# Kernel optimization log

Measured on AMD Instinct MI355X. Metric: run time of the kernel, lower is better.

Reference implementation:

```python
import jax, jax.numpy as jnp
import numpy as np

G = 32; N = G * G          # gridsize, num_nodes per graph
A = 16                      # n_agents
B = 32                      # batch_size
E = 4096                    # edges per graph (~4-neighbor grid)
F_IN = 16                   # input_dim
H = 64                      # hidden_dim
L = 3                       # n_graph_layers
MID = F_IN + L * H          # 208
CAT = 2 * MID + H           # 480
MIN_VAL = -1e8


def _layer_norm(x, g, b, eps=1e-5):
    m = x.mean(-1, keepdims=True)
    v = x.var(-1, keepdims=True)
    return (x - m) * jax.lax.rsqrt(v + eps) * g + b


def setup_inputs() -> dict:
    key = jax.random.key(0)
    ks = jax.random.split(key, 16)
    inp = {}
    inp["graph_nodes"] = jax.random.normal(ks[0], (B, N, F_IN), jnp.float32)
    inp["graph_edge_links"] = jax.random.randint(ks[1], (B, 2, E), 0, N)
    inp["agent_locations"] = jax.random.randint(ks[2], (B, A), 0, N)
    inp["mask"] = jax.random.bernoulli(ks[3], 0.5, (B, A * N))
    inp["dist_matrix"] = jax.random.uniform(ks[4], (N, N), jnp.float32)
    dims = [F_IN] + [H] * L
    k = 5
    for l in range(L):
        inp[f"conv{l}_W"] = jax.random.normal(ks[k], (dims[l], H), jnp.float32) * 0.05
        inp[f"conv{l}_b"] = jnp.zeros((H,), jnp.float32)
        inp[f"conv{l}_g"] = jnp.ones((H,), jnp.float32)
        inp[f"conv{l}_beta"] = jnp.zeros((H,), jnp.float32)
        k += 1
    inp["edges_W"] = jax.random.normal(ks[k], (1, H), jnp.float32) * 0.05
    inp["edges_b"] = jnp.zeros((H,), jnp.float32)
    inp["actor1_W"] = jax.random.normal(ks[k + 1], (CAT, MID), jnp.float32) * 0.05
    inp["actor1_b"] = jnp.zeros((MID,), jnp.float32)
    inp["bn_g"] = jnp.ones((MID,), jnp.float32)
    inp["bn_b"] = jnp.zeros((MID,), jnp.float32)
    inp["actor2_W"] = jax.random.normal(ks[k + 2], (MID, 1), jnp.float32) * 0.05
    inp["actor2_b"] = jnp.zeros((1,), jnp.float32)
    return inp


def reference(graph_nodes, graph_edge_links, agent_locations, mask, dist_matrix,
              conv0_W, conv0_b, conv0_g, conv0_beta,
              conv1_W, conv1_b, conv1_g, conv1_beta,
              conv2_W, conv2_b, conv2_g, conv2_beta,
              edges_W, edges_b, actor1_W, actor1_b, bn_g, bn_b,
              actor2_W, actor2_b):
    # --- batch graphs: offset node indices per graph (Batch.from_data_list) ---
    x = graph_nodes.reshape(B * N, F_IN)
    offs = (jnp.arange(B) * N)[:, None, None]
    ei = (graph_edge_links + offs).transpose(1, 0, 2).reshape(2, B * E)
    src, dst = ei[0], ei[1]

    conv_params = [(conv0_W, conv0_b, conv0_g, conv0_beta),
                   (conv1_W, conv1_b, conv1_g, conv1_beta),
                   (conv2_W, conv2_b, conv2_g, conv2_beta)]
    outs = [x]
    for W, bb, g, beta in conv_params:
        # GINConv with eps=-1: (1+eps)*x_i == 0, so out = mlp(sum_j x_j)
        agg = jax.ops.segment_sum(x[src], dst, num_segments=B * N)
        x = jax.nn.relu(_layer_norm(agg @ W + bb, g, beta))  # mlp relu; outer .relu() idempotent
        outs.append(x)
    xc = jnp.concatenate(outs, axis=1).reshape(B, N, MID)

    # --- all-pairs (agent, node) feature build ---
    a = jnp.take_along_axis(xc, agent_locations[:, :, None], axis=1)  # [B, A, MID]
    a = jnp.repeat(a, N, axis=1)                                      # [B, A*N, MID]
    bfeat = jnp.tile(xc, (1, A, 1))                                   # [B, A*N, MID]
    c = dist_matrix[agent_locations].reshape(B, A * N, 1)             # [B, A*N, 1]
    c = c @ edges_W + edges_b                                         # [B, A*N, H]
    h = jnp.concatenate([a, bfeat, c], axis=2).reshape(-1, CAT)

    h = h @ actor1_W + actor1_b
    mu = h.mean(0)
    var = h.var(0)
    h = (h - mu) * jax.lax.rsqrt(var + 1e-5) * bn_g + bn_b  # BatchNorm1d, training stats
    h = jax.nn.relu(h)
    logits = (h @ actor2_W + actor2_b).reshape(B, A * N)
    logits = jnp.where(mask, logits, MIN_VAL)
    return jax.nn.softmax(logits, axis=1)
```

## Files before the change

kernel.cpp:

```cpp
#include <hip/hip_runtime.h>
#include <cstddef>

#define B_    32
#define N_    1024
#define E_    4096
#define A_    16
#define FIN_  16
#define H_    64
#define MID_  208
#define NODES (B_ * N_)
#define NEDGE (B_ * E_)
#define ROWS  (B_ * A_ * N_)
#define AN_   (A_ * N_)

__device__ __forceinline__ float readlane_f(float v, int l) {
  return __uint_as_float(__builtin_amdgcn_readlane(__float_as_uint(v), l));
}

typedef __attribute__((ext_vector_type(8))) __bf16 bf16x8;
typedef __attribute__((ext_vector_type(4))) float f32x4;

__device__ __forceinline__ f32x4 mfma16(bf16x8 a, bf16x8 b, f32x4 c) {
  return __builtin_amdgcn_mfma_f32_16x16x32_bf16(a, b, c, 0, 0, 0);
}

__device__ __forceinline__ void cvt8(const float* __restrict__ p, bf16x8& hi, bf16x8& lo) {
  float4 v0 = *(const float4*)p;
  float4 v1 = *(const float4*)(p + 4);
  float vv[8] = {v0.x, v0.y, v0.z, v0.w, v1.x, v1.y, v1.z, v1.w};
#pragma unroll
  for (int i = 0; i < 8; i++) {
    __bf16 h = (__bf16)vv[i];
    hi[i] = h;
    lo[i] = (__bf16)(vv[i] - (float)h);
  }
}

__global__ __launch_bounds__(256) void k_front(const int* __restrict__ el,
                                               const float* __restrict__ dist,
                                               const int* __restrict__ loc,
                                               const float* __restrict__ W1,
                                               const float* __restrict__ eW,
                                               const float* __restrict__ eb,
                                               const float* __restrict__ b1,
                                               int* __restrict__ rowptr,
                                               int* __restrict__ counts,
                                               int* __restrict__ ssrc,
                                               float* __restrict__ d1row,
                                               float* __restrict__ c2row,
                                               float* __restrict__ e1,
                                               float* __restrict__ cu,
                                               float* __restrict__ base,
                                               __bf16* __restrict__ W1BTh,
                                               __bf16* __restrict__ W1BTl) {
  __shared__ int cnt[1024];
  __shared__ int cur[1024];
  __shared__ int part[256];
  __shared__ int ssrcS[4096];
  __shared__ int loc_s[16];
  int blk = blockIdx.x, t = threadIdx.x;
  if (blk < 32) {
    int b = blk;
    for (int i = t; i < 1024; i += 256) cnt[i] = 0;
    __syncthreads();
    const int* srcp = el + b * (2 * E_);
    const int* dstp = srcp + E_;
    for (int i = t; i < E_; i += 256) atomicAdd(&cnt[dstp[i]], 1);
    __syncthreads();
    int4 c4 = *(const int4*)&cnt[t * 4];
    int s = c4.x + c4.y + c4.z + c4.w;
    part[t] = s;
    __syncthreads();
    for (int off = 1; off < 256; off <<= 1) {
      int v = (t >= off) ? part[t - off] : 0;
      __syncthreads();
      part[t] += v;
      __syncthreads();
    }
    int prev = (t == 0) ? 0 : part[t - 1];
    int p0 = prev, p1 = p0 + c4.x, p2 = p1 + c4.y, p3 = p2 + c4.z;
    *(int4*)&rowptr[b * 1024 + t * 4] = make_int4(p0 + b * E_, p1 + b * E_, p2 + b * E_, p3 + b * E_);
    *(int4*)&counts[b * 1024 + t * 4] = c4;
    cur[t * 4 + 0] = p0;
    cur[t * 4 + 1] = p1;
    cur[t * 4 + 2] = p2;
    cur[t * 4 + 3] = p3;
    __syncthreads();
    for (int i = t; i < E_; i += 256) {
      int dl = dstp[i];
      int sl = srcp[i];
      int pos = atomicAdd(&cur[dl], 1);
      ssrcS[pos] = b * N_ + sl;
    }
    __syncthreads();
    for (int i = t; i < E_; i += 256) ssrc[b * E_ + i] = ssrcS[i];
  } else if (blk < 288) {
    int lane = t & 63, w = t >> 6;
    int r = (blk - 32) * 4 + w;
    const float* dr = dist + (size_t)r * N_;
    float s = 0.f, c2 = 0.f;
#pragma unroll
    for (int k = 0; k < 16; k++) {
      float v = dr[lane + 64 * k];
      s += v;
      c2 = fmaf(v, v, c2);
    }
#pragma unroll
    for (int o = 32; o > 0; o >>= 1) { s += __shfl_xor(s, o); c2 += __shfl_xor(c2, o); }
    if (lane == 0) { d1row[r] = s; c2row[r] = c2; }
  } else if (blk < 320) {
    int b = blk - 288;
    if (t < 16) loc_s[t] = loc[b * 16 + t];
    __syncthreads();
    float e4[4] = {0.f, 0.f, 0.f, 0.f};
    for (int a = 0; a < 16; a++) {
      const float* dr = dist + (size_t)loc_s[a] * N_;
#pragma unroll
      for (int k = 0; k < 4; k++) e4[k] += dr[t + 256 * k];
    }
#pragma unroll
    for (int k = 0; k < 4; k++) e1[b * N_ + t + 256 * k] = e4[k];
  } else if (blk == 320) {
    int j = t;
    if (j < MID_) {
      float c = 0.f, bs = 0.f;
      for (int k = 0; k < H_; k++) {
        float w = W1[(2 * MID_ + k) * MID_ + j];
        c = fmaf(eW[k], w, c);
        bs = fmaf(eb[k], w, bs);
      }
      cu[j] = c;
      base[j] = bs + b1[j];
    }
  } else {
    int jr = blk - 321;
    if (t < 224) {
      float v = (t < MID_) ? W1[(size_t)(MID_ + t) * MID_ + jr] : 0.f;
      __bf16 h = (__bf16)v;
      W1BTh[jr * 224 + t] = h;
      W1BTl[jr * 224 + t] = (__bf16)(v - (float)h);
    }
  }
}

template <int FINT, bool COPYIN>
__global__ __launch_bounds__(256) void k_layer(const float* __restrict__ xin, int xstride, int in_off,
                                               float* __restrict__ xc, int out_off,
                                               const int* __restrict__ rowptr,
                                               const int* __restrict__ counts,
                                               const int* __restrict__ ssrc,
                                               const float* __restrict__ W,
                                               const float* __restrict__ bias,
                                               const float* __restrict__ g,
                                               const float* __restrict__ beta) {
  int t = threadIdx.x, lane = t & 63, w = t >> 6;
  float Wcol[FINT];
#pragma unroll
  for (int f = 0; f < FINT; f++) Wcol[f] = W[f * 64 + lane];
  float bv = bias[lane], gv = g[lane], bev = beta[lane];
  constexpr int CH = 64 / FINT;
  int f = lane & (FINT - 1);
  int ch = (FINT == 64) ? 0 : (lane >> 4);
  int blk = blockIdx.x;
  int xcd = blk & 7, kk = blk >> 3;
  int graph = xcd * 4 + (kk >> 5);
  int nblk = kk & 31;
  int nbase = graph * N_ + nblk * 32 + w * 8;

  float agg[8];
#pragma unroll
  for (int nn = 0; nn < 8; nn++) {
    int node = nbase + nn;
    int r0 = rowptr[node];
    int deg = counts[node];
    float a0 = 0.f, a1 = 0.f, a2 = 0.f, a3 = 0.f;
    int e = ch;
    for (; e + 3 * CH < deg; e += 4 * CH) {
      int s0 = ssrc[r0 + e];
      int s1 = ssrc[r0 + e + CH];
      int s2 = ssrc[r0 + e + 2 * CH];
      int s3 = ssrc[r0 + e + 3 * CH];
      a0 += xin[(size_t)s0 * xstride + in_off + f];
      a1 += xin[(size_t)s1 * xstride + in_off + f];
      a2 += xin[(size_t)s2 * xstride + in_off + f];
      a3 += xin[(size_t)s3 * xstride + in_off + f];
    }
    for (; e < deg; e += CH) {
      int s = ssrc[r0 + e];
      a0 += xin[(size_t)s * xstride + in_off + f];
    }
    agg[nn] = (a0 + a1) + (a2 + a3);
  }

#pragma unroll
  for (int nn = 0; nn < 8; nn++) {
    int node = nbase + nn;
    float aggf = agg[nn];
    float y0 = bv, y1 = 0.f, y2 = 0.f, y3 = 0.f;
#pragma unroll
    for (int l = 0; l < 64; l += 4) {
      y0 = fmaf(readlane_f(aggf, l + 0), Wcol[(l + 0) & (FINT - 1)], y0);
      y1 = fmaf(readlane_f(aggf, l + 1), Wcol[(l + 1) & (FINT - 1)], y1);
      y2 = fmaf(readlane_f(aggf, l + 2), Wcol[(l + 2) & (FINT - 1)], y2);
      y3 = fmaf(readlane_f(aggf, l + 3), Wcol[(l + 3) & (FINT - 1)], y3);
    }
    float y = (y0 + y1) + (y2 + y3);
    float m = y;
#pragma unroll
    for (int o = 32; o > 0; o >>= 1) m += __shfl_xor(m, o);
    m *= (1.f / 64.f);
    float d = y - m;
    float vv = d * d;
#pragma unroll
    for (int o = 32; o > 0; o >>= 1) vv += __shfl_xor(vv, o);
    vv *= (1.f / 64.f);
    float outv = fmaxf(d * rsqrtf(vv + 1e-5f) * gv + bev, 0.f);
    xc[(size_t)node * MID_ + out_off + lane] = outv;
    if (COPYIN) {
      if (lane < FIN_) xc[(size_t)node * MID_ + lane] = xin[(size_t)node * FIN_ + lane];
    }
  }
}

__global__ __launch_bounds__(256) void k_p1(const float* __restrict__ xc,
                                            const float* __restrict__ W1,
                                            const __bf16* __restrict__ W1BTh,
                                            const __bf16* __restrict__ W1BTl,
                                            const float* __restrict__ e1,
                                            const int* __restrict__ loc,
                                            float* __restrict__ pBT,
                                            float* __restrict__ pA,
                                            float* __restrict__ SB1,
                                            float* __restrict__ SB2,
                                            float* __restrict__ SB3) {
  __shared__ float xr[MID_];
  int t = threadIdx.x, lane = t & 63;
  int w = t >> 6;
  int blk = blockIdx.x;
  if (blk < 1024) {
    int nb = blk * 32;
    int q = lane >> 4, li = lane & 15;
    int jt0 = (w == 0) ? 0 : (w == 1) ? 4 : (w == 2) ? 7 : 10;
    int njt = (w == 0) ? 4 : 3;
    f32x4 zero4 = {0.f, 0.f, 0.f, 0.f};
    f32x4 acc0[4], acc1[4];
#pragma unroll
    for (int i = 0; i < 4; i++) { acc0[i] = zero4; acc1[i] = zero4; }
    const float* xr0 = xc + (size_t)(nb + li) * MID_;
    const float* xr1 = xc + (size_t)(nb + 16 + li) * MID_;
    for (int kc = 0; kc < 7; kc++) {
      int k0 = kc * 32 + q * 8;
      bf16x8 b0h, b0l, b1h, b1l;
      if (k0 < MID_) {
        cvt8(xr0 + k0, b0h, b0l);
        cvt8(xr1 + k0, b1h, b1l);
      } else {
#pragma unroll
        for (int i = 0; i < 8; i++) {
          b0h[i] = (__bf16)0.f; b0l[i] = (__bf16)0.f;
          b1h[i] = (__bf16)0.f; b1l[i] = (__bf16)0.f;
        }
      }
#pragma unroll
      for (int jj = 0; jj < 4; jj++) {
        if (jj < njt) {
          int jt = jt0 + jj;
          bf16x8 ah = *(const bf16x8*)(W1BTh + (size_t)(jt * 16 + li) * 224 + k0);
          bf16x8 al = *(const bf16x8*)(W1BTl + (size_t)(jt * 16 + li) * 224 + k0);
          acc0[jj] = mfma16(ah, b0h, acc0[jj]);
          acc0[jj] = mfma16(ah, b0l, acc0[jj]);
          acc0[jj] = mfma16(al, b0h, acc0[jj]);
          acc1[jj] = mfma16(ah, b1h, acc1[jj]);
          acc1[jj] = mfma16(ah, b1l, acc1[jj]);
          acc1[jj] = mfma16(al, b1h, acc1[jj]);
        }
      }
    }
    float ev0 = e1[nb + li];
    float ev1 = e1[nb + 16 + li];
#pragma unroll
    for (int jj = 0; jj < 4; jj++) {
      if (jj < njt) {
        int jt = jt0 + jj;
#pragma unroll
        for (int r = 0; r < 4; r++) {
          int j = jt * 16 + q * 4 + r;
          float* pb = pBT + (size_t)j * NODES + nb + li;
          pb[0] = acc0[jj][r];
          pb[16] = acc1[jj][r];
        }
        float s1v[4], s2v[4], s3v[4];
#pragma unroll
        for (int r = 0; r < 4; r++) {
          float a0 = acc0[jj][r], a1 = acc1[jj][r];
          s1v[r] = a0 + a1;
          s2v[r] = fmaf(a0, a0, a1 * a1);
          s3v[r] = fmaf(a0, ev0, a1 * ev1);
        }
#pragma unroll
        for (int o = 8; o > 0; o >>= 1) {
#pragma unroll
          for (int r = 0; r < 4; r++) {
            s1v[r] += __shfl_xor(s1v[r], o);
            s2v[r] += __shfl_xor(s2v[r], o);
            s3v[r] += __shfl_xor(s3v[r], o);
          }
        }
        if (li < 4) {
          float g1 = (li == 0) ? s1v[0] : (li == 1) ? s1v[1] : (li == 2) ? s1v[2] : s1v[3];
          float g2 = (li == 0) ? s2v[0] : (li == 1) ? s2v[1] : (li == 2) ? s2v[2] : s2v[3];
          float g3 = (li == 0) ? s3v[0] : (li == 1) ? s3v[1] : (li == 2) ? s3v[2] : s3v[3];
          int j = jt * 16 + q * 4 + li;
          SB1[(size_t)blk * MID_ + j] = g1;
          SB2[(size_t)blk * MID_ + j] = g2;
          SB3[(size_t)blk * MID_ + j] = g3;
        }
      }
    }
  } else {
    int ab = blk - 1024;
    int b = ab >> 4;
    int node = b * N_ + loc[ab];
    for (int i = t; i < MID_; i += 256) xr[i] = xc[(size_t)node * MID_ + i];
    __syncthreads();
    if (t < MID_) {
      float acc = 0.f;
      for (int i = 0; i < MID_; i++) acc = fmaf(xr[i], W1[i * MID_ + t], acc);
      pA[ab * MID_ + t] = acc;
    }
  }
}

__global__ __launch_bounds__(256) void k_fin(const float* __restrict__ SB1,
                                             const float* __restrict__ SB2,
                                             const float* __restrict__ SB3,
                                             const float* __restrict__ pA,
                                             const float* __restrict__ cu,
                                             const float* __restrict__ base,
                                             const float* __restrict__ d1row,
                                             const float* __restrict__ c2row,
                                             const int* __restrict__ loc,
                                             const float* __restrict__ bng,
                                             const float* __restrict__ bnb,
                                             const float* __restrict__ W2,
                                             float* __restrict__ vaT,
                                             float* __restrict__ wpack4) {
  __shared__ float utmp[1536 + 192];
  __shared__ float redm[4];
  __shared__ float reds[4];
  __shared__ float bcast[2];
  int t = threadIdx.x, lane = t & 63, w = t >> 6;
  int j = blockIdx.x;
  float cuj = cu[j], bj = base[j];
  float q1 = 0.f, q2 = 0.f, q3 = 0.f;
#pragma unroll
  for (int c = t * 4; c < t * 4 + 4; c++) {
    q1 += SB1[(size_t)c * MID_ + j];
    q2 += SB2[(size_t)c * MID_ + j];
    q3 += SB3[(size_t)c * MID_ + j];
  }
  float t1 = 0.f, t2 = 0.f, t3 = 0.f;
#pragma unroll
  for (int r = t * 2; r < t * 2 + 2; r++) {
    float pa = pA[r * MID_ + j] + bj;
    t1 += pa;
    t2 = fmaf(pa, pa, t2);
    t3 = fmaf(pa, d1row[loc[r]], t3);
  }
  utmp[0 * 256 + t] = q1;
  utmp[1 * 256 + t] = q2;
  utmp[2 * 256 + t] = q3;
  utmp[3 * 256 + t] = t1;
  utmp[4 * 256 + t] = t2;
  utmp[5 * 256 + t] = t3;
  float p1 = 0.f, p2 = 0.f;
#pragma unroll
  for (int r = t * 2; r < t * 2 + 2; r++) {
    int l = loc[r];
    p1 += d1row[l];
    p2 += c2row[l];
  }
#pragma unroll
  for (int o = 32; o > 0; o >>= 1) { p1 += __shfl_xor(p1, o); p2 += __shfl_xor(p2, o); }
  if (lane == 0) { redm[w] = p1; reds[w] = p2; }
  __syncthreads();
  if (t < 192) {
    int s = t >> 5, b32 = t & 31;
    float ssum = 0.f;
#pragma unroll
    for (int i = 0; i < 8; i++) ssum += utmp[s * 256 + b32 * 8 + i];
    utmp[1536 + s * 32 + b32] = ssum;
  }
  __syncthreads();
  if (t == 0) {
    float Sc1 = (redm[0] + redm[1]) + (redm[2] + redm[3]);
    float Sc2 = (reds[0] + reds[1]) + (reds[2] + reds[3]);
    double T1 = 0, T2 = 0, T3 = 0, cross = 0, sp1 = 0, sp2 = 0, spe = 0;
    for (int b = 0; b < 32; b++) {
      float sq1 = utmp[1536 + 0 * 32 + b];
      float sq2 = utmp[1536 + 1 * 32 + b];
      float sq3 = utmp[1536 + 2 * 32 + b];
      float pt1 = utmp[1536 + 3 * 32 + b];
      float pt2 = utmp[1536 + 4 * 32 + b];
      float pt3 = utmp[1536 + 5 * 32 + b];
      T1 += pt1; T2 += pt2; T3 += pt3;
      cross += (double)pt1 * sq1;
      sp1 += sq1; sp2 += sq2; spe += sq3;
    }
    double s1 = 1024.0 * T1 + 16.0 * sp1 + (double)cuj * Sc1;
    double s2 = 1024.0 * T2 + 16.0 * sp2 + (double)cuj * cuj * Sc2 +
                2.0 * (cross + (double)cuj * (T3 + spe));
    double mu = s1 * (1.0 / (double)ROWS);
    double var = s2 * (1.0 / (double)ROWS) - mu * mu;
    float sc = (float)(1.0 / sqrt(var + 1e-5)) * bng[j];
    float sh = bnb[j] - (float)mu * sc;
    bcast[0] = sc;
    bcast[1] = sh;
    wpack4[4 * j + 0] = sc;
    wpack4[4 * j + 1] = cuj * sc;
    wpack4[4 * j + 2] = W2[j];
    wpack4[4 * j + 3] = 0.f;
  }
  __syncthreads();
  float sc = bcast[0], sh = bcast[1];
#pragma unroll
  for (int r = t * 2; r < t * 2 + 2; r++) {
    int b = r >> 4, a = r & 15;
    float pa = pA[r * MID_ + j] + bj;
    vaT[((size_t)b * MID_ + j) * 16 + a] = pa * sc + sh;
  }
}

__global__ __launch_bounds__(512) void k_logits(const float* __restrict__ pBT,
                                                const float* __restrict__ vaT,
                                                const float* __restrict__ wpack4,
                                                const float* __restrict__ dist,
                                                const int* __restrict__ loc,
                                                const int* __restrict__ mask,
                                                const float* __restrict__ b2,
                                                float* __restrict__ lg,
                                                float2* __restrict__ Psm) {
  __shared__ float vaS[MID_ * 16];
  __shared__ float accL[8][8][64];
  __shared__ int loc_s[16];
  __shared__ float redm[8];
  __shared__ float reds[8];
  int t = threadIdx.x, lane = t & 63;
  int w = __builtin_amdgcn_readfirstlane(t >> 6);
  int b = blockIdx.y, nt = blockIdx.x;
  int n0 = nt * 64;
  if (t < 16) loc_s[t] = loc[b * 16 + t];
  for (int i = t; i < MID_ * 16; i += 512) vaS[i] = vaT[(size_t)b * MID_ * 16 + i];
  __syncthreads();
  float c[16];
#pragma unroll
  for (int a = 0; a < 16; a++) c[a] = dist[(size_t)loc_s[a] * N_ + n0 + lane];
  float acc16[16];
#pragma unroll
  for (int a = 0; a < 16; a++) acc16[a] = 0.f;
  const float4* wp = (const float4*)wpack4;
  int ng = b * N_ + n0 + lane;
  int jb = w * 26;
#pragma unroll 2
  for (int jj = 0; jj < 26; jj++) {
    int j = jb + jj;
    float pbv = pBT[(size_t)j * NODES + ng];
    float4 wv = wp[j];
    float pbs = pbv * wv.x;
    const float* va = &vaS[j * 16];
#pragma unroll
    for (int a = 0; a < 16; a++) {
      float h = fmaf(c[a], wv.y, va[a] + pbs);
      h = fmaxf(h, 0.f);
      acc16[a] = fmaf(h, wv.z, acc16[a]);
    }
  }

  float b2v = b2[0];
  float sv[2];
  int ois[2];
  unsigned mk = 0;
#pragma unroll
  for (int half = 0; half < 2; half++) {
#pragma unroll
    for (int a8 = 0; a8 < 8; a8++) accL[t >> 6][a8][lane] = acc16[half * 8 + a8];
    __syncthreads();
    {
      int a8 = t >> 6, nn = t & 63;
      float s = b2v;
#pragma unroll
      for (int ww = 0; ww < 8; ww++) s += accL[ww][a8][nn];
      int a = half * 8 + a8;
      int oi = b * AN_ + a * N_ + n0 + nn;
      bool m_ = mask[oi] != 0;
      sv[half] = m_ ? s : -1e8f;
      ois[half] = oi;
      mk |= (m_ ? 1u : 0u) << half;
    }
    __syncthreads();
  }

  float mx = fmaxf(sv[0], sv[1]);
#pragma unroll
  for (int o = 32; o > 0; o >>= 1) mx = fmaxf(mx, __shfl_xor(mx, o));
  if (lane == 0) redm[t >> 6] = mx;
  __syncthreads();
  mx = fmaxf(fmaxf(fmaxf(redm[0], redm[1]), fmaxf(redm[2], redm[3])),
             fmaxf(fmaxf(redm[4], redm[5]), fmaxf(redm[6], redm[7])));
  float ssum = 0.f;
#pragma unroll
  for (int iv = 0; iv < 2; iv++) {
    float pv = ((mk >> iv) & 1u) ? expf(sv[iv] - mx) : 0.f;
    lg[ois[iv]] = pv;
    ssum += pv;
  }
#pragma unroll
  for (int o = 32; o > 0; o >>= 1) ssum += __shfl_xor(ssum, o);
  if (lane == 0) reds[t >> 6] = ssum;
  __syncthreads();
  if (t == 0) {
    float S = ((reds[0] + reds[1]) + (reds[2] + reds[3])) +
              ((reds[4] + reds[5]) + (reds[6] + reds[7]));
    Psm[b * 16 + nt] = make_float2(mx, S);
  }
}

__global__ __launch_bounds__(256) void k_sm2(const float* __restrict__ lg,
                                             const float2* __restrict__ P,
                                             float* __restrict__ out) {
  __shared__ float scs[16];
  int b = blockIdx.y, x = blockIdx.x, t = threadIdx.x;
  float M = -3.0e38f;
  float2 pr[16];
#pragma unroll
  for (int k = 0; k < 16; k++) {
    pr[k] = P[b * 16 + k];
    M = fmaxf(M, pr[k].x);
  }
  float S = 0.f;
#pragma unroll
  for (int k = 0; k < 16; k++) S += pr[k].y * expf(pr[k].x - M);
  float inv = 1.0f / S;
  if (t < 16) scs[t] = expf(pr[t].x - M) * inv;
  __syncthreads();
  const float* lb = lg + b * AN_ + x * 2048;
  float* ob = out + b * AN_ + x * 2048;
#pragma unroll
  for (int k = 0; k < 8; k++) {
    int i = t + 256 * k;
    int n = (x * 2048 + i) & 1023;
    ob[i] = lb[i] * scs[n >> 6];
  }
}

extern "C" void kernel_launch(void* const* d_in, const int* in_sizes, int n_in,
                              void* d_out, int out_size, void* d_ws, size_t ws_size,
                              hipStream_t stream) {
  const float* gn = (const float*)d_in[0];
  const int* el = (const int*)d_in[1];
  const int* loc = (const int*)d_in[2];
  const int* mask = (const int*)d_in[3];
  const float* dist = (const float*)d_in[4];
  const float* c0W = (const float*)d_in[5];
  const float* c0b = (const float*)d_in[6];
  const float* c0g = (const float*)d_in[7];
  const float* c0be = (const float*)d_in[8];
  const float* c1W = (const float*)d_in[9];
  const float* c1b = (const float*)d_in[10];
  const float* c1g = (const float*)d_in[11];
  const float* c1be = (const float*)d_in[12];
  const float* c2W = (const float*)d_in[13];
  const float* c2b = (const float*)d_in[14];
  const float* c2g = (const float*)d_in[15];
  const float* c2be = (const float*)d_in[16];
  const float* eW = (const float*)d_in[17];
  const float* eb = (const float*)d_in[18];
  const float* W1 = (const float*)d_in[19];
  const float* b1 = (const float*)d_in[20];
  const float* bng = (const float*)d_in[21];
  const float* bnb = (const float*)d_in[22];
  const float* W2 = (const float*)d_in[23];
  const float* b2 = (const float*)d_in[24];
  float* out = (float*)d_out;

  char* p = (char*)d_ws;
  auto alloc = [&](size_t bytes) {
    char* r = p;
    p += (bytes + 255) & ~(size_t)255;
    return r;
  };
  int* counts = (int*)alloc((size_t)NODES * 4);
  int* rowptr = (int*)alloc((size_t)NODES * 4);
  int* ssrc = (int*)alloc((size_t)NEDGE * 4);
  float* xc = (float*)alloc((size_t)NODES * MID_ * 4);
  float* pBT = (float*)alloc((size_t)NODES * MID_ * 4);
  float* pA = (float*)alloc((size_t)512 * MID_ * 4);
  float* cu = (float*)alloc(256 * 4);
  float* base = (float*)alloc(256 * 4);
  float* d1row = (float*)alloc((size_t)N_ * 4);
  float* c2row = (float*)alloc((size_t)N_ * 4);
  float* e1 = (float*)alloc((size_t)B_ * N_ * 4);
  float* vaT = (float*)alloc((size_t)B_ * MID_ * 16 * 4);
  float* wpack4 = (float*)alloc((size_t)MID_ * 4 * 4);
  float* lg = (float*)alloc((size_t)ROWS * 4);
  float2* Psm = (float2*)alloc((size_t)B_ * 16 * 8);
  __bf16* W1BTh = (__bf16*)alloc((size_t)MID_ * 224 * 2);
  __bf16* W1BTl = (__bf16*)alloc((size_t)MID_ * 224 * 2);
  float* SB1 = (float*)alloc((size_t)1024 * MID_ * 4);
  float* SB2 = (float*)alloc((size_t)1024 * MID_ * 4);
  float* SB3 = (float*)alloc((size_t)1024 * MID_ * 4);

  k_front<<<529, 256, 0, stream>>>(el, dist, loc, W1, eW, eb, b1,
                                   rowptr, counts, ssrc, d1row, c2row, e1, cu, base,
                                   W1BTh, W1BTl);

  k_layer<16, true><<<1024, 256, 0, stream>>>(gn, FIN_, 0, xc, 16, rowptr, counts, ssrc, c0W, c0b, c0g, c0be);
  k_layer<64, false><<<1024, 256, 0, stream>>>(xc, MID_, 16, xc, 80, rowptr, counts, ssrc, c1W, c1b, c1g, c1be);
  k_layer<64, false><<<1024, 256, 0, stream>>>(xc, MID_, 80, xc, 144, rowptr, counts, ssrc, c2W, c2b, c2g, c2be);

  k_p1<<<1536, 256, 0, stream>>>(xc, W1, W1BTh, W1BTl, e1, loc, pBT, pA, SB1, SB2, SB3);
  k_fin<<<208, 256, 0, stream>>>(SB1, SB2, SB3, pA, cu, base, d1row, c2row, loc, bng, bnb, W2, vaT, wpack4);

  k_logits<<<dim3(16, 32), 512, 0, stream>>>(pBT, vaT, wpack4, dist, loc, mask, b2, lg, Psm);
  k_sm2<<<dim3(8, 32), 256, 0, stream>>>(lg, Psm, out);
}
```

Measured before the change: 246.1 us.

## Compute graph-layer dense transform with split-bf16 MFMA instead of readlane FMAs

The per-node 64x64 linear transform in the graph conv layers now runs as bf16 MFMA 16x16x32 with hi/lo splitting (three MFMAs per step) to keep near-fp32 accuracy. Before, each output used a chain of 64 readlane+FMA steps. Weights are transposed and split into bf16 hi/lo in extra k_front blocks. Aggregates are staged through shared memory, each wave now covers 16 nodes, and the grid is halved. LayerNorm and the output writes are vectorised. The cost is the shared staging, extra setup blocks and fewer blocks per layer, which may reduce latency hiding in the gather phase.

```diff
diff --git a/kernel.cpp b/kernel.cpp
--- a/kernel.cpp
+++ b/kernel.cpp
@@ -13,10 +13,6 @@
 #define ROWS  (B_ * A_ * N_)
 #define AN_   (A_ * N_)
 
-__device__ __forceinline__ float readlane_f(float v, int l) {
-  return __uint_as_float(__builtin_amdgcn_readlane(__float_as_uint(v), l));
-}
-
 typedef __attribute__((ext_vector_type(8))) __bf16 bf16x8;
 typedef __attribute__((ext_vector_type(4))) float f32x4;
 
@@ -43,6 +39,9 @@
                                                const float* __restrict__ eW,
                                                const float* __restrict__ eb,
                                                const float* __restrict__ b1,
+                                               const float* __restrict__ c0W,
+                                               const float* __restrict__ c1W,
+                                               const float* __restrict__ c2W,
                                                int* __restrict__ rowptr,
                                                int* __restrict__ counts,
                                                int* __restrict__ ssrc,
@@ -52,7 +51,9 @@
                                                float* __restrict__ cu,
                                                float* __restrict__ base,
                                                __bf16* __restrict__ W1BTh,
-                                               __bf16* __restrict__ W1BTl) {
+                                               __bf16* __restrict__ W1BTl,
+                                               __bf16* __restrict__ WTh,
+                                               __bf16* __restrict__ WTl) {
   __shared__ int cnt[1024];
   __shared__ int cur[1024];
   __shared__ int part[256];
@@ -132,7 +133,7 @@
       cu[j] = c;
       base[j] = bs + b1[j];
     }
-  } else {
+  } else if (blk < 529) {
     int jr = blk - 321;
     if (t < 224) {
       float v = (t < MID_) ? W1[(size_t)(MID_ + t) * MID_ + jr] : 0.f;
@@ -140,6 +141,17 @@
       W1BTh[jr * 224 + t] = h;
       W1BTl[jr * 224 + t] = (__bf16)(v - (float)h);
     }
+  } else {
+    int l = blk - 529;
+    const float* Wsrc = (l == 0) ? c0W : (l == 1) ? c1W : c2W;
+    int fmask = (l == 0) ? 15 : 63;
+    for (int i = t; i < 4096; i += 256) {
+      int j = i >> 6, k = i & 63;
+      float v = Wsrc[(k & fmask) * 64 + j];
+      __bf16 h = (__bf16)v;
+      WTh[l * 4096 + j * 64 + k] = h;
+      WTl[l * 4096 + j * 64 + k] = (__bf16)(v - (float)h);
+    }
   }
 }
 
@@ -149,28 +161,26 @@
                                                const int* __restrict__ rowptr,
                                                const int* __restrict__ counts,
                                                const int* __restrict__ ssrc,
-                                               const float* __restrict__ W,
+                                               const __bf16* __restrict__ WTh,
+                                               const __bf16* __restrict__ WTl,
                                                const float* __restrict__ bias,
                                                const float* __restrict__ g,
                                                const float* __restrict__ beta) {
+  __shared__ float aggS[4][16][68];
   int t = threadIdx.x, lane = t & 63, w = t >> 6;
-  float Wcol[FINT];
-#pragma unroll
-  for (int f = 0; f < FINT; f++) Wcol[f] = W[f * 64 + lane];
-  float bv = bias[lane], gv = g[lane], bev = beta[lane];
   constexpr int CH = 64 / FINT;
   int f = lane & (FINT - 1);
   int ch = (FINT == 64) ? 0 : (lane >> 4);
   int blk = blockIdx.x;
   int xcd = blk & 7, kk = blk >> 3;
-  int graph = xcd * 4 + (kk >> 5);
-  int nblk = kk & 31;
-  int nbase = graph * N_ + nblk * 32 + w * 8;
-
-  float agg[8];
-#pragma unroll
-  for (int nn = 0; nn < 8; nn++) {
-    int node = nbase + nn;
+  int graph = xcd * 4 + (kk >> 4);
+  int nblk = kk & 15;
+  int tilebase = graph * N_ + nblk * 64 + w * 16;
+
+  float aggv[16];
+#pragma unroll
+  for (int nn = 0; nn < 16; nn++) {
+    int node = tilebase + nn;
     int r0 = rowptr[node];
     int deg = counts[node];
     float a0 = 0.f, a1 = 0.f, a2 = 0.f, a3 = 0.f;
@@ -189,36 +199,72 @@
       int s = ssrc[r0 + e];
       a0 += xin[(size_t)s * xstride + in_off + f];
     }
-    agg[nn] = (a0 + a1) + (a2 + a3);
-  }
-
-#pragma unroll
-  for (int nn = 0; nn < 8; nn++) {
-    int node = nbase + nn;
-    float aggf = agg[nn];
-    float y0 = bv, y1 = 0.f, y2 = 0.f, y3 = 0.f;
-#pragma unroll
-    for (int l = 0; l < 64; l += 4) {
-      y0 = fmaf(readlane_f(aggf, l + 0), Wcol[(l + 0) & (FINT - 1)], y0);
-      y1 = fmaf(readlane_f(aggf, l + 1), Wcol[(l + 1) & (FINT - 1)], y1);
-      y2 = fmaf(readlane_f(aggf, l + 2), Wcol[(l + 2) & (FINT - 1)], y2);
-      y3 = fmaf(readlane_f(aggf, l + 3), Wcol[(l + 3) & (FINT - 1)], y3);
-    }
-    float y = (y0 + y1) + (y2 + y3);
-    float m = y;
-#pragma unroll
-    for (int o = 32; o > 0; o >>= 1) m += __shfl_xor(m, o);
-    m *= (1.f / 64.f);
-    float d = y - m;
-    float vv = d * d;
-#pragma unroll
-    for (int o = 32; o > 0; o >>= 1) vv += __shfl_xor(vv, o);
-    vv *= (1.f / 64.f);
-    float outv = fmaxf(d * rsqrtf(vv + 1e-5f) * gv + bev, 0.f);
-    xc[(size_t)node * MID_ + out_off + lane] = outv;
-    if (COPYIN) {
-      if (lane < FIN_) xc[(size_t)node * MID_ + lane] = xin[(size_t)node * FIN_ + lane];
-    }
+    aggv[nn] = (a0 + a1) + (a2 + a3);
+  }
+#pragma unroll
+  for (int nn = 0; nn < 16; nn++) aggS[w][nn][lane] = aggv[nn];
+
+  int q = lane >> 4, li = lane & 15;
+  bf16x8 bh[2], bl[2];
+#pragma unroll
+  for (int ks = 0; ks < 2; ks++) cvt8(&aggS[w][li][ks * 32 + q * 8], bh[ks], bl[ks]);
+
+  f32x4 zero4 = {0.f, 0.f, 0.f, 0.f};
+  f32x4 acc[4];
+#pragma unroll
+  for (int jt = 0; jt < 4; jt++) {
+    acc[jt] = zero4;
+#pragma unroll
+    for (int ks = 0; ks < 2; ks++) {
+      bf16x8 ah = *(const bf16x8*)(WTh + (size_t)(jt * 16 + li) * 64 + ks * 32 + q * 8);
+      bf16x8 al = *(const bf16x8*)(WTl + (size_t)(jt * 16 + li) * 64 + ks * 32 + q * 8);
+      acc[jt] = mfma16(ah, bh[ks], acc[jt]);
+      acc[jt] = mfma16(ah, bl[ks], acc[jt]);
+      acc[jt] = mfma16(al, bh[ks], acc[jt]);
+    }
+  }
+
+  float y[16];
+#pragma unroll
+  for (int jt = 0; jt < 4; jt++) {
+    float4 b4 = *(const float4*)(bias + jt * 16 + q * 4);
+    y[jt * 4 + 0] = acc[jt][0] + b4.x;
+    y[jt * 4 + 1] = acc[jt][1] + b4.y;
+    y[jt * 4 + 2] = acc[jt][2] + b4.z;
+    y[jt * 4 + 3] = acc[jt][3] + b4.w;
+  }
+  float s = 0.f;
+#pragma unroll
+  for (int i = 0; i < 16; i++) s += y[i];
+  s += __shfl_xor(s, 16);
+  s += __shfl_xor(s, 32);
+  float m = s * (1.f / 64.f);
+  float vv = 0.f;
+#pragma unroll
+  for (int i = 0; i < 16; i++) {
+    float d = y[i] - m;
+    vv = fmaf(d, d, vv);
+  }
+  vv += __shfl_xor(vv, 16);
+  vv += __shfl_xor(vv, 32);
+  float rs = rsqrtf(vv * (1.f / 64.f) + 1e-5f);
+
+  size_t node = tilebase + li;
+  float* xrow = xc + node * MID_ + out_off;
+#pragma unroll
+  for (int jt = 0; jt < 4; jt++) {
+    float4 g4 = *(const float4*)(g + jt * 16 + q * 4);
+    float4 be4 = *(const float4*)(beta + jt * 16 + q * 4);
+    float4 o;
+    o.x = fmaxf((y[jt * 4 + 0] - m) * rs * g4.x + be4.x, 0.f);
+    o.y = fmaxf((y[jt * 4 + 1] - m) * rs * g4.y + be4.y, 0.f);
+    o.z = fmaxf((y[jt * 4 + 2] - m) * rs * g4.z + be4.z, 0.f);
+    o.w = fmaxf((y[jt * 4 + 3] - m) * rs * g4.w + be4.w, 0.f);
+    *(float4*)(xrow + jt * 16 + q * 4) = o;
+  }
+  if (COPYIN) {
+    float4 v = *(const float4*)(xin + node * FIN_ + q * 4);
+    *(float4*)(xc + node * MID_ + q * 4) = v;
   }
 }
 
@@ -609,14 +655,19 @@
   float* SB1 = (float*)alloc((size_t)1024 * MID_ * 4);
   float* SB2 = (float*)alloc((size_t)1024 * MID_ * 4);
   float* SB3 = (float*)alloc((size_t)1024 * MID_ * 4);
-
-  k_front<<<529, 256, 0, stream>>>(el, dist, loc, W1, eW, eb, b1,
+  __bf16* WTh = (__bf16*)alloc((size_t)3 * 4096 * 2);
+  __bf16* WTl = (__bf16*)alloc((size_t)3 * 4096 * 2);
+
+  k_front<<<532, 256, 0, stream>>>(el, dist, loc, W1, eW, eb, b1, c0W, c1W, c2W,
                                    rowptr, counts, ssrc, d1row, c2row, e1, cu, base,
-                                   W1BTh, W1BTl);
-
-  k_layer<16, true><<<1024, 256, 0, stream>>>(gn, FIN_, 0, xc, 16, rowptr, counts, ssrc, c0W, c0b, c0g, c0be);
-  k_layer<64, false><<<1024, 256, 0, stream>>>(xc, MID_, 16, xc, 80, rowptr, counts, ssrc, c1W, c1b, c1g, c1be);
-  k_layer<64, false><<<1024, 256, 0, stream>>>(xc, MID_, 80, xc, 144, rowptr, counts, ssrc, c2W, c2b, c2g, c2be);
+                                   W1BTh, W1BTl, WTh, WTl);
+
+  k_layer<16, true><<<512, 256, 0, stream>>>(gn, FIN_, 0, xc, 16, rowptr, counts, ssrc,
+                                             WTh, WTl, c0b, c0g, c0be);
+  k_layer<64, false><<<512, 256, 0, stream>>>(xc, MID_, 16, xc, 80, rowptr, counts, ssrc,
+                                              WTh + 4096, WTl + 4096, c1b, c1g, c1be);
+  k_layer<64, false><<<512, 256, 0, stream>>>(xc, MID_, 80, xc, 144, rowptr, counts, ssrc,
+                                              WTh + 8192, WTl + 8192, c2b, c2g, c2be);
 
   k_p1<<<1536, 256, 0, stream>>>(xc, W1, W1BTh, W1BTl, e1, loc, pBT, pA, SB1, SB2, SB3);
   k_fin<<<208, 256, 0, stream>>>(SB1, SB2, SB3, pA, cu, base, d1row, c2row, loc, bng, bnb, W2, vaT, wpack4);
```

New measurement: 249.7 us. No clear change (+1.5%).
